# Kernel optimization log

Hardware: AMD Instinct MI355X
Metric: run time of the kernel (lower is better)

## Reference

```python
import jax, jax.numpy as jnp
import numpy as np

B, S, HID = 2, 1024, 4096
NH, NKV, D = 32, 8, 128
G = NH // NKV            # query heads per KV head (GQA group size)
WINDOW = 512             # sliding window
ROPE_BASE = 10000.0
NEG = -1e30


def setup_inputs() -> dict:
    key = jax.random.key(0)
    k0, k1, k2, k3, k4 = jax.random.split(key, 5)
    hidden_states = jax.random.normal(k0, (B, S, HID), jnp.float32)
    # rotate-half RoPE tables, width = head_dim
    inv_freq = 1.0 / (ROPE_BASE ** (jnp.arange(0, D, 2, dtype=jnp.float32) / D))
    freqs = jnp.outer(jnp.arange(S, dtype=jnp.float32), inv_freq)
    emb = jnp.concatenate([freqs, freqs], axis=-1)  # [S, D]
    cos, sin = jnp.cos(emb), jnp.sin(emb)
    qkv_out = (NH + 2 * NKV) * D  # fused QKV: 6144
    w_qkv = jax.random.normal(k1, (qkv_out, HID), jnp.float32) / np.sqrt(HID).astype(np.float32)
    b_qkv = jax.random.normal(k2, (qkv_out,), jnp.float32) * 0.01
    w_o = jax.random.normal(k3, (HID, NH * D), jnp.float32) / np.sqrt(NH * D).astype(np.float32)
    b_o = jax.random.normal(k4, (HID,), jnp.float32) * 0.01
    return dict(hidden_states=hidden_states, cos=cos, sin=sin,
                w_qkv=w_qkv, b_qkv=b_qkv, w_o=w_o, b_o=b_o)


def _rotate_half(x):
    x1, x2 = jnp.split(x, 2, axis=-1)
    return jnp.concatenate([-x2, x1], axis=-1)


def reference(hidden_states, cos, sin, w_qkv, b_qkv, w_o, b_o):
    # fused QKV projection (with bias, per attention_bias=True)
    qkv = jnp.einsum('bsh,oh->bso', hidden_states, w_qkv) + b_qkv
    q = qkv[..., : NH * D].reshape(B, S, NKV, G, D)
    k = qkv[..., NH * D : (NH + NKV) * D].reshape(B, S, NKV, D)
    v = qkv[..., (NH + NKV) * D :].reshape(B, S, NKV, D)
    # rotate-half RoPE
    c = cos[None, :, None, :]  # [1,S,1,D]
    s = sin[None, :, None, :]
    q = q * c[..., None, :] + _rotate_half(q) * s[..., None, :]
    k = k * c + _rotate_half(k) * s
    # GQA attention: scores [B, NKV, G, Sq, Sk]
    scores = jnp.einsum('bqkgd,bskd->bkgqs', q, k) / np.sqrt(D).astype(np.float32)
    i = jnp.arange(S)[:, None]
    j = jnp.arange(S)[None, :]
    mask = (j <= i) & (i - j < WINDOW)  # causal + sliding window
    scores = jnp.where(mask, scores, NEG)
    p = jax.nn.softmax(scores, axis=-1)
    attn = jnp.einsum('bkgqs,bskd->bqkgd', p, v).reshape(B, S, NH * D)
    return jnp.einsum('bsd,hd->bsh', attn, w_o) + b_o
```

## Files before the change

kernel.cpp:

```cpp
#include <hip/hip_runtime.h>
#include <hip/hip_bf16.h>

#define B_      2
#define S_      1024
#define HID     4096
#define NH      32
#define NKV     8
#define D_      128
#define G_      4
#define WINDOW  512
#define QKV_OUT 6144
#define M_TOT   2048
#define CH      32
#define VSTR    40

typedef __bf16 bf16x8 __attribute__((ext_vector_type(8)));
typedef float  f32x4  __attribute__((ext_vector_type(4)));
typedef unsigned short u16x8 __attribute__((ext_vector_type(8)));

#define AS1 __attribute__((address_space(1)))
#define AS3 __attribute__((address_space(3)))

static __device__ __forceinline__ float bf2f(unsigned short u) {
    union { unsigned int i; float f; } v; v.i = ((unsigned int)u) << 16; return v.f;
}
static __device__ __forceinline__ unsigned short f2bf(float f) {
    union { float f; unsigned int i; } v; v.f = f;
    unsigned int x = v.i;
    return (unsigned short)((x + 0x7fffu + ((x >> 16) & 1u)) >> 16);
}
static __device__ __forceinline__ void gl2lds16(const void* g, void* l) {
    __builtin_amdgcn_global_load_lds((const AS1 void*)g, (AS3 void*)l, 16, 0, 0);
}

__global__ __launch_bounds__(256)
void conv_f32_bf16(const float* __restrict__ src, unsigned short* __restrict__ dst, int n8)
{
    int i = blockIdx.x * 256 + threadIdx.x;
    if (i >= n8) return;
    const float* p = src + (size_t)i * 8;
    float4 f0 = *(const float4*)p;
    float4 f1 = *(const float4*)(p + 4);
    u16x8 h;
    h[0]=f2bf(f0.x); h[1]=f2bf(f0.y); h[2]=f2bf(f0.z); h[3]=f2bf(f0.w);
    h[4]=f2bf(f1.x); h[5]=f2bf(f1.y); h[6]=f2bf(f1.z); h[7]=f2bf(f1.w);
    *(u16x8*)&dst[(size_t)i * 8] = h;
}

#define MFMA_PAIR(MT0, MT1, AR)                                                        \
    __builtin_amdgcn_s_setprio(1);                                                    \
    _Pragma("unroll")                                                                  \
    for (int ks = 0; ks < 2; ++ks) {                                                   \
        _Pragma("unroll")                                                              \
        for (int nt = 0; nt < 4; ++nt) {                                               \
            acc[MT0][nt] = __builtin_amdgcn_mfma_f32_16x16x32_bf16(AR[0][ks], bC[nt][ks], acc[MT0][nt], 0, 0, 0); \
            acc[MT1][nt] = __builtin_amdgcn_mfma_f32_16x16x32_bf16(AR[1][ks], bC[nt][ks], acc[MT1][nt], 0, 0, 0); \
        }                                                                              \
    }                                                                                  \
    __builtin_amdgcn_s_setprio(0);

#define SCHED __builtin_amdgcn_sched_barrier(0)
#define WAITLGKM(N) do { asm volatile("s_waitcnt lgkmcnt(" #N ")" ::: "memory"); SCHED; } while (0)
#define BARRIER do { SCHED; __builtin_amdgcn_s_barrier(); SCHED; } while (0)

template<bool C_BF16>
__global__ __launch_bounds__(512, 2)
void gemm256_8ph(const unsigned short* __restrict__ A,
                 const unsigned short* __restrict__ Bw,
                 const float* __restrict__ bias,
                 void* __restrict__ Cv,
                 int M, int N, int K)
{
    __shared__ __attribute__((aligned(1024))) unsigned short lds[65536];

    const int tid  = threadIdx.x;
    const int lane = tid & 63;
    const int w    = tid >> 6;
    const int m_   = w >> 2;
    const int n_   = w & 3;
    const int lm   = lane & 15, quad = lane >> 4;
    const int m0   = blockIdx.y * 256, n0 = blockIdx.x * 256;
    const int nkt  = K >> 6;

    const int srow = lane >> 3;
    const int scol = ((lane & 7) ^ srow) * 8;

    const int arow0 = m0 + m_ * 128 + n_ * 16;
    const int arow1 = arow0 + 64;
    const int brow  = n0 + w * 32;

    const int ldsAr = m_ * 8192;
    const int ldsA0 = ldsAr + n_ * 1024;
    const int ldsA1 = ldsA0 + 4096;
    const int ldsBs = 32768 + m_ * 8192 + n_ * 2048;
    const int ldsBr = 32768 + (n_ >> 1) * 8192 + (n_ & 1) * 4096;

    f32x4 acc[8][4] = {};
    bf16x8 bC[4][2];
    bf16x8 aP[2][2], aQ[2][2];

    auto stA = [&](int T, int rp) {
        const int k0   = T << 6;
        const int bufo = (T & 1) << 14;
        const int rb   = (rp ? arow1 : arow0) + srow;
        const int lb   = (rp ? ldsA1 : ldsA0) + bufo + lane * 8;
        gl2lds16(&A[(size_t)rb * K + k0 + scol],       &lds[lb]);
        gl2lds16(&A[(size_t)(rb + 8) * K + k0 + scol], &lds[lb + 512]);
    };
    auto stB = [&](int T, int pr) {
        const int k0   = T << 6;
        const int bufo = (T & 1) << 14;
        const int rb   = brow + pr * 16 + srow;
        const int lb   = ldsBs + pr * 1024 + bufo + lane * 8;
        gl2lds16(&Bw[(size_t)rb * K + k0 + scol],       &lds[lb]);
        gl2lds16(&Bw[(size_t)(rb + 8) * K + k0 + scol], &lds[lb + 512]);
    };
    auto rdA = [&](int bufo, int mt, int ks) -> bf16x8 {
        int e = (mt * 16 + lm) * 64 + ks * 32 + quad * 8;
        e ^= ((e >> 6) & 7) << 3;
        return *(const bf16x8*)&lds[bufo + ldsAr + e];
    };
    auto rdB = [&](int bufo, int nt, int ks) -> bf16x8 {
        int e = (nt * 16 + lm) * 64 + ks * 32 + quad * 8;
        e ^= ((e >> 6) & 7) << 3;
        return *(const bf16x8*)&lds[bufo + ldsBr + e];
    };
    auto rdBoundary = [&](int T) {
        const int bufo = (T & 1) << 14;
        #pragma unroll
        for (int nt = 0; nt < 4; ++nt)
            #pragma unroll
            for (int ks = 0; ks < 2; ++ks) bC[nt][ks] = rdB(bufo, nt, ks);
        #pragma unroll
        for (int ks = 0; ks < 2; ++ks) { aP[0][ks] = rdA(bufo, 0, ks); aP[1][ks] = rdA(bufo, 1, ks); }
    };

    stB(0, 0); stB(0, 1); stA(0, 0); stA(0, 1);
    stB(1, 0); stB(1, 1); stA(1, 0);
    asm volatile("s_waitcnt vmcnt(6)" ::: "memory");
    BARRIER;
    rdBoundary(0);
    SCHED;

    #pragma unroll 1
    for (int i = 0; i < nkt; ++i) {
        const int bufo = (i & 1) << 14;
        if (i + 1 < nkt) stA(i + 1, 1);
        #pragma unroll
        for (int ks = 0; ks < 2; ++ks) { aQ[0][ks] = rdA(bufo, 2, ks); aQ[1][ks] = rdA(bufo, 3, ks); }
        SCHED;
        WAITLGKM(4);
        MFMA_PAIR(0, 1, aP)
        BARRIER;
        if (i + 2 < nkt) stB(i + 2, 0);
        #pragma unroll
        for (int ks = 0; ks < 2; ++ks) { aP[0][ks] = rdA(bufo, 4, ks); aP[1][ks] = rdA(bufo, 5, ks); }
        SCHED;
        WAITLGKM(4);
        MFMA_PAIR(2, 3, aQ)
        BARRIER;
        if (i + 2 < nkt) stB(i + 2, 1);
        #pragma unroll
        for (int ks = 0; ks < 2; ++ks) { aQ[0][ks] = rdA(bufo, 6, ks); aQ[1][ks] = rdA(bufo, 7, ks); }
        SCHED;
        WAITLGKM(4);
        MFMA_PAIR(4, 5, aP)
        BARRIER;
        if (i + 2 < nkt) stA(i + 2, 0);
        SCHED;
        WAITLGKM(0);
        MFMA_PAIR(6, 7, aQ)
        SCHED;
        if (i + 2 < nkt)      { asm volatile("s_waitcnt vmcnt(6)" ::: "memory"); }
        else if (i + 1 < nkt) { asm volatile("s_waitcnt vmcnt(0)" ::: "memory"); }
        BARRIER;
        if (i + 1 < nkt) rdBoundary(i + 1);
        SCHED;
    }

    #pragma unroll
    for (int nt = 0; nt < 4; ++nt) {
        const int col = n0 + n_ * 64 + nt * 16 + lm;
        const float bv = bias[col];
        #pragma unroll
        for (int mt = 0; mt < 8; ++mt) {
            const int rowb = m0 + m_ * 128 + mt * 16 + quad * 4;
            #pragma unroll
            for (int r = 0; r < 4; ++r) {
                const float val = acc[mt][nt][r] + bv;
                if (C_BF16)
                    ((unsigned short*)Cv)[(size_t)(rowb + r) * N + col] = f2bf(val);
                else
                    ((float*)Cv)[(size_t)(rowb + r) * N + col] = val;
            }
        }
    }
}

template<bool C_BF16>
__global__ __launch_bounds__(256)
void gemm_bf16_bt(const unsigned short* __restrict__ A,
                  const unsigned short* __restrict__ Bw,
                  const float* __restrict__ bias,
                  void* __restrict__ Cv,
                  int M, int N, int K)
{
    __shared__ unsigned short As[128 * 32];
    __shared__ unsigned short Bs[128 * 32];

    const int tid  = threadIdx.x;
    const int m0   = blockIdx.y * 128;
    const int n0   = blockIdx.x * 128;
    const int wave = tid >> 6, lane = tid & 63;
    const int wm   = (wave >> 1) * 64;
    const int wn   = (wave & 1) * 64;
    const int lm   = lane & 15, quad = lane >> 4;

    f32x4 acc[4][4] = {};

    for (int k0 = 0; k0 < K; k0 += 32) {
        __syncthreads();
        #pragma unroll
        for (int p = 0; p < 2; ++p) {
            int chunk = tid + p * 256;
            int row   = chunk >> 2;
            int off   = (chunk & 3) * 8;
            gl2lds16(&A [(size_t)(m0 + row) * K + k0 + off], &As[chunk * 8]);
            gl2lds16(&Bw[(size_t)(n0 + row) * K + k0 + off], &Bs[chunk * 8]);
        }
        __syncthreads();

        bf16x8 afr[4], bfr[4];
        #pragma unroll
        for (int i = 0; i < 4; ++i)
            afr[i] = *(const bf16x8*)&As[(wm + i * 16 + lm) * 32 + quad * 8];
        #pragma unroll
        for (int j = 0; j < 4; ++j)
            bfr[j] = *(const bf16x8*)&Bs[(wn + j * 16 + lm) * 32 + quad * 8];

        #pragma unroll
        for (int i = 0; i < 4; ++i)
            #pragma unroll
            for (int j = 0; j < 4; ++j)
                acc[i][j] = __builtin_amdgcn_mfma_f32_16x16x32_bf16(afr[i], bfr[j], acc[i][j], 0, 0, 0);
    }

    #pragma unroll
    for (int j = 0; j < 4; ++j) {
        int col = n0 + wn + j * 16 + lm;
        float bv = bias[col];
        #pragma unroll
        for (int i = 0; i < 4; ++i) {
            int rowb = m0 + wm + i * 16 + quad * 4;
            #pragma unroll
            for (int r = 0; r < 4; ++r) {
                float val = acc[i][j][r] + bv;
                if (C_BF16)
                    ((unsigned short*)Cv)[(size_t)(rowb + r) * N + col] = f2bf(val);
                else
                    ((float*)Cv)[(size_t)(rowb + r) * N + col] = val;
            }
        }
    }
}

template<bool A_BF16, bool C_BF16>
__global__ __launch_bounds__(256)
void gemm_bt_bias(const void* __restrict__ Av,
                  const float* __restrict__ Bw,
                  const float* __restrict__ bias,
                  void* __restrict__ Cv,
                  int M, int N, int K)
{
    __shared__ unsigned short As[128 * 40];
    __shared__ unsigned short Bs[128 * 40];

    const int tid  = threadIdx.x;
    const int m0   = blockIdx.y * 128;
    const int n0   = blockIdx.x * 128;
    const int wave = tid >> 6, lane = tid & 63;
    const int wm   = (wave >> 1) * 64;
    const int wn   = (wave & 1) * 64;
    const int lm   = lane & 15, quad = lane >> 4;

    f32x4 acc[4][4] = {};

    for (int k0 = 0; k0 < K; k0 += 32) {
        __syncthreads();
        #pragma unroll
        for (int c = 0; c < 2; ++c) {
            int chunk = tid + c * 256;
            int row   = chunk >> 2;
            int off   = (chunk & 3) * 8;
            if (A_BF16) {
                *(u16x8*)&As[row * 40 + off] =
                    *(const u16x8*)&((const unsigned short*)Av)[(size_t)(m0 + row) * K + k0 + off];
            } else {
                const float* ap = &((const float*)Av)[(size_t)(m0 + row) * K + k0 + off];
                float4 f0 = *(const float4*)ap;
                float4 f1 = *(const float4*)(ap + 4);
                u16x8 h;
                h[0]=f2bf(f0.x); h[1]=f2bf(f0.y); h[2]=f2bf(f0.z); h[3]=f2bf(f0.w);
                h[4]=f2bf(f1.x); h[5]=f2bf(f1.y); h[6]=f2bf(f1.z); h[7]=f2bf(f1.w);
                *(u16x8*)&As[row * 40 + off] = h;
            }
            {
                const float* bp = &Bw[(size_t)(n0 + row) * K + k0 + off];
                float4 f0 = *(const float4*)bp;
                float4 f1 = *(const float4*)(bp + 4);
                u16x8 h;
                h[0]=f2bf(f0.x); h[1]=f2bf(f0.y); h[2]=f2bf(f0.z); h[3]=f2bf(f0.w);
                h[4]=f2bf(f1.x); h[5]=f2bf(f1.y); h[6]=f2bf(f1.z); h[7]=f2bf(f1.w);
                *(u16x8*)&Bs[row * 40 + off] = h;
            }
        }
        __syncthreads();

        bf16x8 afr[4], bfr[4];
        #pragma unroll
        for (int i = 0; i < 4; ++i)
            afr[i] = *(const bf16x8*)&As[(wm + i * 16 + lm) * 40 + quad * 8];
        #pragma unroll
        for (int j = 0; j < 4; ++j)
            bfr[j] = *(const bf16x8*)&Bs[(wn + j * 16 + lm) * 40 + quad * 8];

        #pragma unroll
        for (int i = 0; i < 4; ++i)
            #pragma unroll
            for (int j = 0; j < 4; ++j)
                acc[i][j] = __builtin_amdgcn_mfma_f32_16x16x32_bf16(afr[i], bfr[j], acc[i][j], 0, 0, 0);
    }

    #pragma unroll
    for (int j = 0; j < 4; ++j) {
        int col = n0 + wn + j * 16 + lm;
        float bv = bias[col];
        #pragma unroll
        for (int i = 0; i < 4; ++i) {
            int rowb = m0 + wm + i * 16 + quad * 4;
            #pragma unroll
            for (int r = 0; r < 4; ++r) {
                float val = acc[i][j][r] + bv;
                if (C_BF16)
                    ((unsigned short*)Cv)[(size_t)(rowb + r) * N + col] = f2bf(val);
                else
                    ((float*)Cv)[(size_t)(rowb + r) * N + col] = val;
            }
        }
    }
}

__global__ __launch_bounds__(256)
void rope_kernel(unsigned short* __restrict__ qkv,
                 const float* __restrict__ cosb,
                 const float* __restrict__ sinb)
{
    int t    = blockIdx.x * 256 + threadIdx.x;
    int d    = t & 63;
    int rest = t >> 6;
    int head = rest % 40;
    int m    = rest / 40;
    int s    = m & (S_ - 1);
    int obase = (head < NH) ? head * D_ : HID + (head - NH) * D_;
    size_t base = (size_t)m * QKV_OUT + obase;

    float x1 = bf2f(qkv[base + d]);
    float x2 = bf2f(qkv[base + d + 64]);
    float c1 = cosb[s * D_ + d];
    float s1 = sinb[s * D_ + d];
    float c2 = cosb[s * D_ + d + 64];
    float s2 = sinb[s * D_ + d + 64];
    qkv[base + d]      = f2bf(x1 * c1 - x2 * s1);
    qkv[base + d + 64] = f2bf(x2 * c2 + x1 * s2);
}

__global__ __launch_bounds__(256)
void attn_mfma(const unsigned short* __restrict__ qkv,
               unsigned short* __restrict__ attn)
{
    __shared__ unsigned short Kl[CH * 136];
    __shared__ unsigned short Vt[128 * VSTR];
    __shared__ unsigned short Pl[4][16 * 40];

    const int tid  = threadIdx.x;
    const int wave = tid >> 6, lane = tid & 63;
    const int lm   = lane & 15, quad = lane >> 4;
    const int h    = blockIdx.y;
    const int b    = blockIdx.z;
    const int kvh  = h >> 2;
    const int r0b  = blockIdx.x * 64;
    const int rw0  = r0b + wave * 16;

    const size_t qkv_b = (size_t)b * S_ * QKV_OUT;
    const float SCL = 0.12751974f;

    bf16x8 qf[4];
    {
        const unsigned short* qrow = qkv + qkv_b + (size_t)(rw0 + lm) * QKV_OUT + h * D_ + quad * 8;
        #pragma unroll
        for (int kb = 0; kb < 4; ++kb)
            qf[kb] = *(const bf16x8*)(qrow + kb * 32);
    }

    f32x4 O[8] = {};
    float mrow[4] = {-1e30f, -1e30f, -1e30f, -1e30f};
    float lrow[4] = {0.f, 0.f, 0.f, 0.f};

    const int c0   = max(0, r0b - (WINDOW - 1)) & ~(CH - 1);
    const int cend = r0b + 64 - CH;

    for (int c = c0; c <= cend; c += CH) {
        __syncthreads();
        #pragma unroll
        for (int p = 0; p < 2; ++p) {
            int idx = tid + p * 256;
            int row = idx >> 4;
            int d0  = (idx & 15) * 8;
            *(u16x8*)&Kl[row * 136 + d0] =
                *(const u16x8*)(qkv + qkv_b + (size_t)(c + row) * QKV_OUT + HID + kvh * D_ + d0);
        }
        {
            int r2 = (tid & 15) * 2;
            int d0 = (tid >> 4) * 8;
            const unsigned short* vg = qkv + qkv_b + (size_t)(c + r2) * QKV_OUT + HID + NKV * D_ + kvh * D_ + d0;
            u16x8 va = *(const u16x8*)vg;
            u16x8 vb = *(const u16x8*)(vg + QKV_OUT);
            #pragma unroll
            for (int e = 0; e < 8; ++e) {
                unsigned int pack = (unsigned int)va[e] | ((unsigned int)vb[e] << 16);
                *(unsigned int*)&Vt[(d0 + e) * VSTR + r2] = pack;
            }
        }
        __syncthreads();

        if (c + CH - 1 < rw0 - (WINDOW - 1) || c > rw0 + 15) continue;

        f32x4 s0 = {}, s1 = {};
        #pragma unroll
        for (int kb = 0; kb < 4; ++kb) {
            bf16x8 b0 = *(const bf16x8*)&Kl[lm * 136 + kb * 32 + quad * 8];
            bf16x8 b1 = *(const bf16x8*)&Kl[(16 + lm) * 136 + kb * 32 + quad * 8];
            s0 = __builtin_amdgcn_mfma_f32_16x16x32_bf16(qf[kb], b0, s0, 0, 0, 0);
            s1 = __builtin_amdgcn_mfma_f32_16x16x32_bf16(qf[kb], b1, s1, 0, 0, 0);
        }

        const int j0 = c + lm, j1 = c + 16 + lm;
        float alpha[4];
        #pragma unroll
        for (int r = 0; r < 4; ++r) {
            int row = rw0 + quad * 4 + r;
            float t0 = (j0 <= row && row - j0 < WINDOW) ? s0[r] : -3.0e38f;
            float t1 = (j1 <= row && row - j1 < WINDOW) ? s1[r] : -3.0e38f;
            float cm = fmaxf(t0, t1);
            #pragma unroll
            for (int o = 8; o >= 1; o >>= 1) cm = fmaxf(cm, __shfl_xor(cm, o, 16));
            float mnew = fmaxf(mrow[r], cm);
            float al   = exp2f((mrow[r] - mnew) * SCL);
            float p0   = exp2f((t0 - mnew) * SCL);
            float p1   = exp2f((t1 - mnew) * SCL);
            float rs   = p0 + p1;
            #pragma unroll
            for (int o = 8; o >= 1; o >>= 1) rs += __shfl_xor(rs, o, 16);
            mrow[r] = mnew;
            lrow[r] = lrow[r] * al + rs;
            alpha[r] = al;
            Pl[wave][(quad * 4 + r) * 40 + lm]      = f2bf(p0);
            Pl[wave][(quad * 4 + r) * 40 + 16 + lm] = f2bf(p1);
        }

        #pragma unroll
        for (int nt = 0; nt < 8; ++nt)
            #pragma unroll
            for (int r = 0; r < 4; ++r)
                O[nt][r] *= alpha[r];

        bf16x8 pa = *(const bf16x8*)&Pl[wave][lm * 40 + quad * 8];
        #pragma unroll
        for (int nt = 0; nt < 8; ++nt) {
            bf16x8 vbf = *(const bf16x8*)&Vt[(nt * 16 + lm) * VSTR + quad * 8];
            O[nt] = __builtin_amdgcn_mfma_f32_16x16x32_bf16(pa, vbf, O[nt], 0, 0, 0);
        }
    }

    float il[4];
    #pragma unroll
    for (int r = 0; r < 4; ++r) il[r] = 1.0f / lrow[r];
    #pragma unroll
    for (int nt = 0; nt < 8; ++nt)
        #pragma unroll
        for (int r = 0; r < 4; ++r) {
            int row = rw0 + quad * 4 + r;
            attn[(size_t)(b * S_ + row) * (NH * D_) + h * D_ + nt * 16 + lm] = f2bf(O[nt][r] * il[r]);
        }
}

extern "C" void kernel_launch(void* const* d_in, const int* in_sizes, int n_in,
                              void* d_out, int out_size, void* d_ws, size_t ws_size,
                              hipStream_t stream)
{
    const float* hidden = (const float*)d_in[0];
    const float* cosb   = (const float*)d_in[1];
    const float* sinb   = (const float*)d_in[2];
    const float* w_qkv  = (const float*)d_in[3];
    const float* b_qkv  = (const float*)d_in[4];
    const float* w_o    = (const float*)d_in[5];
    const float* b_o    = (const float*)d_in[6];
    float* out = (float*)d_out;

    unsigned char* ws = (unsigned char*)d_ws;
    const size_t QKV_B  = (size_t)M_TOT * QKV_OUT * 2;
    const size_t ATTN_B = (size_t)M_TOT * HID * 2;
    const size_t HB_B   = (size_t)M_TOT * HID * 2;
    const size_t WQ_B   = (size_t)QKV_OUT * HID * 2;
    const size_t WO_B   = (size_t)HID * HID * 2;
    const size_t NEED   = QKV_B + ATTN_B + HB_B + WQ_B;

    unsigned short* qkv_ws  = (unsigned short*)(ws);
    unsigned short* attn_ws = (unsigned short*)(ws + QKV_B);

    dim3 blk(256);

    if (ws_size >= NEED && WO_B <= HB_B + WQ_B) {
        unsigned short* hb = (unsigned short*)(ws + QKV_B + ATTN_B);
        unsigned short* wq = (unsigned short*)(ws + QKV_B + ATTN_B + HB_B);
        unsigned short* wo = (unsigned short*)(ws + QKV_B + ATTN_B);

        int n8h = M_TOT * HID / 8;
        int n8q = QKV_OUT * HID / 8;
        int n8o = HID * HID / 8;
        conv_f32_bf16<<<dim3((n8h + 255) / 256), blk, 0, stream>>>(hidden, hb, n8h);
        conv_f32_bf16<<<dim3((n8q + 255) / 256), blk, 0, stream>>>(w_qkv, wq, n8q);
        gemm256_8ph<true><<<dim3(QKV_OUT / 256, M_TOT / 256), dim3(512), 0, stream>>>(
            hb, wq, b_qkv, qkv_ws, M_TOT, QKV_OUT, HID);
        rope_kernel<<<dim3((M_TOT * 40 * 64) / 256), blk, 0, stream>>>(qkv_ws, cosb, sinb);
        conv_f32_bf16<<<dim3((n8o + 255) / 256), blk, 0, stream>>>(w_o, wo, n8o);
        attn_mfma<<<dim3(S_ / 64, NH, B_), blk, 0, stream>>>(qkv_ws, attn_ws);
        gemm_bf16_bt<false><<<dim3(HID / 128, M_TOT / 128), blk, 0, stream>>>(
            attn_ws, wo, b_o, out, M_TOT, HID, NH * D_);
    } else {
        gemm_bt_bias<false, true><<<dim3(QKV_OUT / 128, M_TOT / 128), blk, 0, stream>>>(
            hidden, w_qkv, b_qkv, qkv_ws, M_TOT, QKV_OUT, HID);
        rope_kernel<<<dim3((M_TOT * 40 * 64) / 256), blk, 0, stream>>>(qkv_ws, cosb, sinb);
        attn_mfma<<<dim3(S_ / 64, NH, B_), blk, 0, stream>>>(qkv_ws, attn_ws);
        gemm_bt_bias<true, false><<<dim3(HID / 128, M_TOT / 128), blk, 0, stream>>>(
            attn_ws, w_o, b_o, out, M_TOT, HID, NH * D_);
    }
}
```

Baseline: 538.9 us.

## Double-buffer B fragments in registers to overlap boundary LDS reads with MFMAs

Gives the GEMM two sets of B-fragment registers that alternate between K-tiles, with the loop unrolled by two. The next tile's B and A fragments are read from LDS before the last MFMA group of the current tile, so those reads overlap compute instead of sitting on a separate boundary. Two of the per-tile barriers are removed and the vmcnt waits are retuned to match. This raises register pressure at 512 threads with 2 blocks per CU, and the unroll by two assumes an even K-tile count (K=4096 gives 64 tiles).

```diff
diff --git a/kernel.cpp b/kernel.cpp
--- a/kernel.cpp
+++ b/kernel.cpp
@@ -47,14 +47,14 @@
     *(u16x8*)&dst[(size_t)i * 8] = h;
 }
 
-#define MFMA_PAIR(MT0, MT1, AR)                                                        \
-    __builtin_amdgcn_s_setprio(1);                                                    \
+#define MFMA_CL(MT0, MT1, AR, BS)                                                      \
+    __builtin_amdgcn_s_setprio(1);                                                     \
     _Pragma("unroll")                                                                  \
     for (int ks = 0; ks < 2; ++ks) {                                                   \
         _Pragma("unroll")                                                              \
         for (int nt = 0; nt < 4; ++nt) {                                               \
-            acc[MT0][nt] = __builtin_amdgcn_mfma_f32_16x16x32_bf16(AR[0][ks], bC[nt][ks], acc[MT0][nt], 0, 0, 0); \
-            acc[MT1][nt] = __builtin_amdgcn_mfma_f32_16x16x32_bf16(AR[1][ks], bC[nt][ks], acc[MT1][nt], 0, 0, 0); \
+            acc[MT0][nt] = __builtin_amdgcn_mfma_f32_16x16x32_bf16(AR[0][ks], BS[nt][ks], acc[MT0][nt], 0, 0, 0); \
+            acc[MT1][nt] = __builtin_amdgcn_mfma_f32_16x16x32_bf16(AR[1][ks], BS[nt][ks], acc[MT1][nt], 0, 0, 0); \
         }                                                                              \
     }                                                                                  \
     __builtin_amdgcn_s_setprio(0);
@@ -62,6 +62,55 @@
 #define SCHED __builtin_amdgcn_sched_barrier(0)
 #define WAITLGKM(N) do { asm volatile("s_waitcnt lgkmcnt(" #N ")" ::: "memory"); SCHED; } while (0)
 #define BARRIER do { SCHED; __builtin_amdgcn_s_barrier(); SCHED; } while (0)
+
+#define RDBOUND(T, BS) do {                                                            \
+    const int bufo_ = ((T) & 1) << 14;                                                 \
+    _Pragma("unroll")                                                                  \
+    for (int nt = 0; nt < 4; ++nt)                                                     \
+        _Pragma("unroll")                                                              \
+        for (int ks = 0; ks < 2; ++ks) BS[nt][ks] = rdB(bufo_, nt, ks);                \
+    _Pragma("unroll")                                                                  \
+    for (int ks = 0; ks < 2; ++ks) { aP[0][ks] = rdA(bufo_, 0, ks); aP[1][ks] = rdA(bufo_, 1, ks); } \
+} while (0)
+
+#define TILE_BODY(II, BOLD, BNEW) do {                                                 \
+    const int i_ = (II);                                                               \
+    const int bufo = (i_ & 1) << 14;                                                   \
+                                   \
+    if (i_ + 1 < nkt) stA(i_ + 1, 1);                                                  \
+    _Pragma("unroll")                                                                  \
+    for (int ks = 0; ks < 2; ++ks) { aQ[0][ks] = rdA(bufo, 2, ks); aQ[1][ks] = rdA(bufo, 3, ks); } \
+    SCHED; WAITLGKM(4);                                                                \
+    MFMA_CL(0, 1, aP, BOLD)                                                            \
+    BARRIER;                                                                           \
+                  \
+    if (i_ + 2 < nkt) stB(i_ + 2, 0);                                                  \
+    _Pragma("unroll")                                                                  \
+    for (int ks = 0; ks < 2; ++ks) { aP[0][ks] = rdA(bufo, 4, ks); aP[1][ks] = rdA(bufo, 5, ks); } \
+    SCHED; WAITLGKM(4);                                                                \
+    MFMA_CL(2, 3, aQ, BOLD)                                                            \
+                  \
+    if (i_ + 2 < nkt) stB(i_ + 2, 1);                                                  \
+    _Pragma("unroll")                                                                  \
+    for (int ks = 0; ks < 2; ++ks) { aQ[0][ks] = rdA(bufo, 6, ks); aQ[1][ks] = rdA(bufo, 7, ks); } \
+    SCHED; WAITLGKM(4);                                                                \
+    MFMA_CL(4, 5, aP, BOLD)                                                            \
+    SCHED;                                                                             \
+             \
+    if (i_ + 1 < nkt) {                                                                \
+        if (i_ + 2 < nkt) { asm volatile("s_waitcnt vmcnt(4)" ::: "memory"); }         \
+        else              { asm volatile("s_waitcnt vmcnt(0)" ::: "memory"); }         \
+        BARRIER;                                                                       \
+        if (i_ + 2 < nkt) stA(i_ + 2, 0);                                              \
+        RDBOUND(i_ + 1, BNEW);                                                         \
+        SCHED; WAITLGKM(12);                                                           \
+        MFMA_CL(6, 7, aQ, BOLD)                                                        \
+        BARRIER;                                                                       \
+    } else {                                                                           \
+        WAITLGKM(0);                                                                   \
+        MFMA_CL(6, 7, aQ, BOLD)                                                        \
+    }                                                                                  \
+} while (0)
 
 template<bool C_BF16>
 __global__ __launch_bounds__(512, 2)
@@ -96,7 +145,7 @@
     const int ldsBr = 32768 + (n_ >> 1) * 8192 + (n_ & 1) * 4096;
 
     f32x4 acc[8][4] = {};
-    bf16x8 bC[4][2];
+    bf16x8 bCA[4][2], bCB[4][2];
     bf16x8 aP[2][2], aQ[2][2];
 
     auto stA = [&](int T, int rp) {
@@ -125,57 +174,18 @@
         e ^= ((e >> 6) & 7) << 3;
         return *(const bf16x8*)&lds[bufo + ldsBr + e];
     };
-    auto rdBoundary = [&](int T) {
-        const int bufo = (T & 1) << 14;
-        #pragma unroll
-        for (int nt = 0; nt < 4; ++nt)
-            #pragma unroll
-            for (int ks = 0; ks < 2; ++ks) bC[nt][ks] = rdB(bufo, nt, ks);
-        #pragma unroll
-        for (int ks = 0; ks < 2; ++ks) { aP[0][ks] = rdA(bufo, 0, ks); aP[1][ks] = rdA(bufo, 1, ks); }
-    };
 
     stB(0, 0); stB(0, 1); stA(0, 0); stA(0, 1);
     stB(1, 0); stB(1, 1); stA(1, 0);
     asm volatile("s_waitcnt vmcnt(6)" ::: "memory");
     BARRIER;
-    rdBoundary(0);
+    RDBOUND(0, bCA);
     SCHED;
 
     #pragma unroll 1
-    for (int i = 0; i < nkt; ++i) {
-        const int bufo = (i & 1) << 14;
-        if (i + 1 < nkt) stA(i + 1, 1);
-        #pragma unroll
-        for (int ks = 0; ks < 2; ++ks) { aQ[0][ks] = rdA(bufo, 2, ks); aQ[1][ks] = rdA(bufo, 3, ks); }
-        SCHED;
-        WAITLGKM(4);
-        MFMA_PAIR(0, 1, aP)
-        BARRIER;
-        if (i + 2 < nkt) stB(i + 2, 0);
-        #pragma unroll
-        for (int ks = 0; ks < 2; ++ks) { aP[0][ks] = rdA(bufo, 4, ks); aP[1][ks] = rdA(bufo, 5, ks); }
-        SCHED;
-        WAITLGKM(4);
-        MFMA_PAIR(2, 3, aQ)
-        BARRIER;
-        if (i + 2 < nkt) stB(i + 2, 1);
-        #pragma unroll
-        for (int ks = 0; ks < 2; ++ks) { aQ[0][ks] = rdA(bufo, 6, ks); aQ[1][ks] = rdA(bufo, 7, ks); }
-        SCHED;
-        WAITLGKM(4);
-        MFMA_PAIR(4, 5, aP)
-        BARRIER;
-        if (i + 2 < nkt) stA(i + 2, 0);
-        SCHED;
-        WAITLGKM(0);
-        MFMA_PAIR(6, 7, aQ)
-        SCHED;
-        if (i + 2 < nkt)      { asm volatile("s_waitcnt vmcnt(6)" ::: "memory"); }
-        else if (i + 1 < nkt) { asm volatile("s_waitcnt vmcnt(0)" ::: "memory"); }
-        BARRIER;
-        if (i + 1 < nkt) rdBoundary(i + 1);
-        SCHED;
+    for (int ii = 0; ii < nkt; ii += 2) {
+        TILE_BODY(ii,     bCA, bCB);
+        TILE_BODY(ii + 1, bCB, bCA);
     }
 
     #pragma unroll
```

New measurement: 1.068 ms. 98.1% more time.

## Shrink QKV GEMM tile to 256x192 and drop two intra-iteration barriers

Applied to the files above, without the earlier changes.

The QKV projection GEMM now uses 256x192 output tiles instead of 256x256. The grid grows from 24x8 to 32x8 blocks, which spreads work better across the CUs, and LDS use and accumulator registers both shrink. B-tile staging is reworked for 24 rows per wave with one fewer global-to-LDS load, and the vmcnt waits and LDS offsets are adjusted to match. Two barriers inside the k-loop are removed. This risks LDS races if the overlapping buffer regions are not actually safe to reuse without them.

```diff
diff --git a/kernel.cpp b/kernel.cpp
--- a/kernel.cpp
+++ b/kernel.cpp
@@ -47,12 +47,12 @@
     *(u16x8*)&dst[(size_t)i * 8] = h;
 }
 
-#define MFMA_PAIR(MT0, MT1, AR)                                                        \
-    __builtin_amdgcn_s_setprio(1);                                                    \
+#define MFMA_CL(MT0, MT1, AR)                                                          \
+    __builtin_amdgcn_s_setprio(1);                                                     \
     _Pragma("unroll")                                                                  \
     for (int ks = 0; ks < 2; ++ks) {                                                   \
         _Pragma("unroll")                                                              \
-        for (int nt = 0; nt < 4; ++nt) {                                               \
+        for (int nt = 0; nt < 3; ++nt) {                                               \
             acc[MT0][nt] = __builtin_amdgcn_mfma_f32_16x16x32_bf16(AR[0][ks], bC[nt][ks], acc[MT0][nt], 0, 0, 0); \
             acc[MT1][nt] = __builtin_amdgcn_mfma_f32_16x16x32_bf16(AR[1][ks], bC[nt][ks], acc[MT1][nt], 0, 0, 0); \
         }                                                                              \
@@ -71,7 +71,7 @@
                  void* __restrict__ Cv,
                  int M, int N, int K)
 {
-    __shared__ __attribute__((aligned(1024))) unsigned short lds[65536];
+    __shared__ __attribute__((aligned(1024))) unsigned short lds[57344];
 
     const int tid  = threadIdx.x;
     const int lane = tid & 63;
@@ -79,7 +79,7 @@
     const int m_   = w >> 2;
     const int n_   = w & 3;
     const int lm   = lane & 15, quad = lane >> 4;
-    const int m0   = blockIdx.y * 256, n0 = blockIdx.x * 256;
+    const int m0   = blockIdx.y * 256, n0 = blockIdx.x * 192;
     const int nkt  = K >> 6;
 
     const int srow = lane >> 3;
@@ -87,16 +87,16 @@
 
     const int arow0 = m0 + m_ * 128 + n_ * 16;
     const int arow1 = arow0 + 64;
-    const int brow  = n0 + w * 32;
+    const int brow  = n0 + w * 24;
 
     const int ldsAr = m_ * 8192;
     const int ldsA0 = ldsAr + n_ * 1024;
     const int ldsA1 = ldsA0 + 4096;
-    const int ldsBs = 32768 + m_ * 8192 + n_ * 2048;
-    const int ldsBr = 32768 + (n_ >> 1) * 8192 + (n_ & 1) * 4096;
-
-    f32x4 acc[8][4] = {};
-    bf16x8 bC[4][2];
+    const int ldsBs = 32768 + w * 1536;
+    const int ldsBr = 32768 + n_ * 3072;
+
+    f32x4 acc[8][3] = {};
+    bf16x8 bC[3][2];
     bf16x8 aP[2][2], aQ[2][2];
 
     auto stA = [&](int T, int rp) {
@@ -109,69 +109,66 @@
     };
     auto stB = [&](int T, int pr) {
         const int k0   = T << 6;
-        const int bufo = (T & 1) << 14;
+        const int bufo = (T & 1) * 12288;
         const int rb   = brow + pr * 16 + srow;
         const int lb   = ldsBs + pr * 1024 + bufo + lane * 8;
-        gl2lds16(&Bw[(size_t)rb * K + k0 + scol],       &lds[lb]);
-        gl2lds16(&Bw[(size_t)(rb + 8) * K + k0 + scol], &lds[lb + 512]);
+        gl2lds16(&Bw[(size_t)rb * K + k0 + scol], &lds[lb]);
+        if (pr == 0)
+            gl2lds16(&Bw[(size_t)(rb + 8) * K + k0 + scol], &lds[lb + 512]);
     };
-    auto rdA = [&](int bufo, int mt, int ks) -> bf16x8 {
+    auto rdA = [&](int T, int mt, int ks) -> bf16x8 {
         int e = (mt * 16 + lm) * 64 + ks * 32 + quad * 8;
         e ^= ((e >> 6) & 7) << 3;
-        return *(const bf16x8*)&lds[bufo + ldsAr + e];
+        return *(const bf16x8*)&lds[((T & 1) << 14) + ldsAr + e];
     };
-    auto rdB = [&](int bufo, int nt, int ks) -> bf16x8 {
+    auto rdB = [&](int T, int nt, int ks) -> bf16x8 {
         int e = (nt * 16 + lm) * 64 + ks * 32 + quad * 8;
         e ^= ((e >> 6) & 7) << 3;
-        return *(const bf16x8*)&lds[bufo + ldsBr + e];
+        return *(const bf16x8*)&lds[(T & 1) * 12288 + ldsBr + e];
     };
     auto rdBoundary = [&](int T) {
-        const int bufo = (T & 1) << 14;
-        #pragma unroll
-        for (int nt = 0; nt < 4; ++nt)
-            #pragma unroll
-            for (int ks = 0; ks < 2; ++ks) bC[nt][ks] = rdB(bufo, nt, ks);
-        #pragma unroll
-        for (int ks = 0; ks < 2; ++ks) { aP[0][ks] = rdA(bufo, 0, ks); aP[1][ks] = rdA(bufo, 1, ks); }
+        #pragma unroll
+        for (int nt = 0; nt < 3; ++nt)
+            #pragma unroll
+            for (int ks = 0; ks < 2; ++ks) bC[nt][ks] = rdB(T, nt, ks);
+        #pragma unroll
+        for (int ks = 0; ks < 2; ++ks) { aP[0][ks] = rdA(T, 0, ks); aP[1][ks] = rdA(T, 1, ks); }
     };
 
     stB(0, 0); stB(0, 1); stA(0, 0); stA(0, 1);
     stB(1, 0); stB(1, 1); stA(1, 0);
-    asm volatile("s_waitcnt vmcnt(6)" ::: "memory");
+    asm volatile("s_waitcnt vmcnt(5)" ::: "memory");
     BARRIER;
     rdBoundary(0);
     SCHED;
 
     #pragma unroll 1
     for (int i = 0; i < nkt; ++i) {
-        const int bufo = (i & 1) << 14;
         if (i + 1 < nkt) stA(i + 1, 1);
         #pragma unroll
-        for (int ks = 0; ks < 2; ++ks) { aQ[0][ks] = rdA(bufo, 2, ks); aQ[1][ks] = rdA(bufo, 3, ks); }
+        for (int ks = 0; ks < 2; ++ks) { aQ[0][ks] = rdA(i, 2, ks); aQ[1][ks] = rdA(i, 3, ks); }
         SCHED;
         WAITLGKM(4);
-        MFMA_PAIR(0, 1, aP)
+        MFMA_CL(0, 1, aP)
         BARRIER;
         if (i + 2 < nkt) stB(i + 2, 0);
         #pragma unroll
-        for (int ks = 0; ks < 2; ++ks) { aP[0][ks] = rdA(bufo, 4, ks); aP[1][ks] = rdA(bufo, 5, ks); }
+        for (int ks = 0; ks < 2; ++ks) { aP[0][ks] = rdA(i, 4, ks); aP[1][ks] = rdA(i, 5, ks); }
         SCHED;
         WAITLGKM(4);
-        MFMA_PAIR(2, 3, aQ)
-        BARRIER;
+        MFMA_CL(2, 3, aQ)
         if (i + 2 < nkt) stB(i + 2, 1);
         #pragma unroll
-        for (int ks = 0; ks < 2; ++ks) { aQ[0][ks] = rdA(bufo, 6, ks); aQ[1][ks] = rdA(bufo, 7, ks); }
+        for (int ks = 0; ks < 2; ++ks) { aQ[0][ks] = rdA(i, 6, ks); aQ[1][ks] = rdA(i, 7, ks); }
         SCHED;
         WAITLGKM(4);
-        MFMA_PAIR(4, 5, aP)
-        BARRIER;
+        MFMA_CL(4, 5, aP)
         if (i + 2 < nkt) stA(i + 2, 0);
         SCHED;
         WAITLGKM(0);
-        MFMA_PAIR(6, 7, aQ)
+        MFMA_CL(6, 7, aQ)
         SCHED;
-        if (i + 2 < nkt)      { asm volatile("s_waitcnt vmcnt(6)" ::: "memory"); }
+        if (i + 2 < nkt)      { asm volatile("s_waitcnt vmcnt(5)" ::: "memory"); }
         else if (i + 1 < nkt) { asm volatile("s_waitcnt vmcnt(0)" ::: "memory"); }
         BARRIER;
         if (i + 1 < nkt) rdBoundary(i + 1);
@@ -179,8 +176,8 @@
     }
 
     #pragma unroll
-    for (int nt = 0; nt < 4; ++nt) {
-        const int col = n0 + n_ * 64 + nt * 16 + lm;
+    for (int nt = 0; nt < 3; ++nt) {
+        const int col = n0 + n_ * 48 + nt * 16 + lm;
         const float bv = bias[col];
         #pragma unroll
         for (int mt = 0; mt < 8; ++mt) {
@@ -530,7 +527,7 @@
         int n8o = HID * HID / 8;
         conv_f32_bf16<<<dim3((n8h + 255) / 256), blk, 0, stream>>>(hidden, hb, n8h);
         conv_f32_bf16<<<dim3((n8q + 255) / 256), blk, 0, stream>>>(w_qkv, wq, n8q);
-        gemm256_8ph<true><<<dim3(QKV_OUT / 256, M_TOT / 256), dim3(512), 0, stream>>>(
+        gemm256_8ph<true><<<dim3(QKV_OUT / 192, M_TOT / 256), dim3(512), 0, stream>>>(
             hb, wq, b_qkv, qkv_ws, M_TOT, QKV_OUT, HID);
         rope_kernel<<<dim3((M_TOT * 40 * 64) / 256), blk, 0, stream>>>(qkv_ws, cosb, sinb);
         conv_f32_bf16<<<dim3((n8o + 255) / 256), blk, 0, stream>>>(w_o, wo, n8o);
```

Result: faster. 517.6 us (-3.9%).
